# Kernel optimization log

Hardware: AMD Instinct MI355X
Metric: run time of the kernel (lower is better)

The kernel has to match this reference:

```python
import jax, jax.numpy as jnp
import numpy as np

B, N, C = 8, 4096, 64          # graphs, points per graph, feature dim
RATIO = 0.25
M = int(N * RATIO)             # 1024 sampled centroids per graph
R = 0.2                        # radius (points live in the unit cube)
K = 64                         # max_num_neighbors in the forward
BIG = 1e10


def fps_single(pos):
    """Farthest point sampling on one cloud. pos: [N,3] -> [M] local indices.
    Deterministic start at index 0 (PyG uses a random start; math is identical)."""
    n = pos.shape[0]

    def step(carry, _):
        mind, last = carry
        d = jnp.sum((pos - pos[last]) ** 2, axis=-1)      # [N]
        mind = jnp.minimum(mind, d)
        nxt = jnp.argmax(mind)
        return (mind, nxt), nxt

    init = (jnp.full((n,), BIG, pos.dtype), jnp.int32(0))
    _, rest = jax.lax.scan(step, init, None, length=M - 1)
    return jnp.concatenate([jnp.zeros((1,), rest.dtype), rest])


def setup_inputs() -> dict:
    key = jax.random.key(0)
    ks = jax.random.split(key, 8)
    x = jax.random.normal(ks[0], (B * N, C), dtype=jnp.float32)
    pos = jax.random.uniform(ks[1], (B * N, 3), dtype=jnp.float32)
    batch = jnp.repeat(jnp.arange(B, dtype=jnp.int64), N)
    seed_idx = jnp.arange(B * N, dtype=jnp.int64)
    d_in, h, f_out = C + 3, 128, 256
    W1 = jax.random.normal(ks[2], (d_in, h), dtype=jnp.float32) / np.sqrt(d_in)
    b1 = jnp.zeros((h,), jnp.float32)
    W2 = jax.random.normal(ks[3], (h, h), dtype=jnp.float32) / np.sqrt(h)
    b2 = jnp.zeros((h,), jnp.float32)
    W3 = jax.random.normal(ks[4], (h, f_out), dtype=jnp.float32) / np.sqrt(h)
    b3 = jnp.zeros((f_out,), jnp.float32)
    return {"x": x, "pos": pos, "batch": batch, "seed_idx": seed_idx,
            "W1": W1, "b1": b1, "W2": W2, "b2": b2, "W3": W3, "b3": b3}


def reference(x, pos, batch, seed_idx, W1, b1, W2, b2, W3, b3):
    posb = pos.reshape(B, N, 3)
    xb = x.reshape(B, N, C)

    # --- FPS per graph (batch is block-contiguous with N points per graph) ---
    idx_local = jax.vmap(fps_single)(posb)                     # [B, M]
    ctr = jax.vmap(lambda p, i: p[i])(posb, idx_local)         # [B, M, 3]

    # --- radius neighbor search: up to K neighbors within r of each centroid ---
    d2 = jnp.sum((ctr[:, :, None, :] - posb[:, None, :, :]) ** 2, axis=-1)  # [B,M,N]
    d2m = jnp.where(d2 < R * R, d2, BIG)
    neg_d, nbr = jax.lax.top_k(-d2m, K)                        # K nearest within r
    valid = (-neg_d) < R * R                                   # [B, M, K]

    # --- PointConv: msg = MLP([x_j, pos_j - pos_i]), max-aggregate ---
    x_j = jax.vmap(lambda a, i: a[i])(xb, nbr)                 # [B, M, K, C]
    pos_j = jax.vmap(lambda p, i: p[i])(posb, nbr)             # [B, M, K, 3]
    msg = jnp.concatenate([x_j, pos_j - ctr[:, :, None, :]], axis=-1)  # [B,M,K,C+3]
    h = jax.nn.relu(msg @ W1 + b1)
    h = jax.nn.relu(h @ W2 + b2)
    h = jax.nn.relu(h @ W3 + b3)                               # [B, M, K, 256]
    h = jnp.where(valid[..., None], h, -BIG)
    out = jnp.max(h, axis=2)                                   # [B, M, 256]
    out = jnp.where(jnp.any(valid, axis=-1)[..., None], out, 0.0)

    # --- gather sampled outputs back to the flat layout ---
    idx_flat = (idx_local + jnp.arange(B)[:, None] * N).reshape(-1)  # [B*M]
    x_out = out.reshape(B * M, -1)
    pos_out = pos[idx_flat]
    batch_out = batch[idx_flat]
    seed_out = seed_idx[idx_flat]
    return x_out, pos_out, batch_out, seed_out
```

## Files before the change

kernel.cpp:

```cpp
#include <hip/hip_runtime.h>
#include <stdint.h>

#define BB 8
#define NN 4096
#define CC 64
#define MM 1024
#define EE (BB*MM)
#define KK 64
#define F3 256
#define SM 104
#define SH 136
#define CAP 768

typedef __bf16 bf16x8 __attribute__((ext_vector_type(8)));
typedef float floatx4 __attribute__((ext_vector_type(4)));

#define DPP_MAXSTEP(ctrl, rmask) { \
    unsigned o = (unsigned)__builtin_amdgcn_update_dpp(0, (int)v, ctrl, rmask, 0xf, false); \
    v = v > o ? v : o; }
__device__ __forceinline__ unsigned wave_umax_u32(unsigned v) {
  DPP_MAXSTEP(0x111, 0xf)
  DPP_MAXSTEP(0x112, 0xf)
  DPP_MAXSTEP(0x114, 0xf)
  DPP_MAXSTEP(0x118, 0xf)
  DPP_MAXSTEP(0x142, 0xa)
  DPP_MAXSTEP(0x143, 0xc)
  return (unsigned)__builtin_amdgcn_readlane((int)v, 63);
}
#define DPP_MINSTEP(ctrl, rmask) { \
    unsigned o = (unsigned)__builtin_amdgcn_update_dpp((int)0xffffffffu, (int)v, ctrl, rmask, 0xf, false); \
    v = v < o ? v : o; }
__device__ __forceinline__ unsigned wave_umin_u32(unsigned v) {
  DPP_MINSTEP(0x111, 0xf)
  DPP_MINSTEP(0x112, 0xf)
  DPP_MINSTEP(0x114, 0xf)
  DPP_MINSTEP(0x118, 0xf)
  DPP_MINSTEP(0x142, 0xa)
  DPP_MINSTEP(0x143, 0xc)
  return (unsigned)__builtin_amdgcn_readlane((int)v, 63);
}

__device__ __forceinline__ void mlp_item(
    int e, int b, int t,
    const float* __restrict__ x, const float4* __restrict__ pos4,
    const float* __restrict__ ctr, const int* __restrict__ fpsIdx,
    const __bf16* __restrict__ W1t, const __bf16* __restrict__ W2t,
    const __bf16* __restrict__ W3t,
    const float* __restrict__ b1, const float* __restrict__ b2,
    const float* __restrict__ b3,
    float* __restrict__ outX, float* __restrict__ outP,
    float* __restrict__ outB, float* __restrict__ outS,
    __bf16* sMsg, __bf16* sH, int* sSel, int* sCnt) {
  unsigned long long* sDI = (unsigned long long*)sMsg;
  const int lane = t & 63, wv = t >> 6;

  const float cx = ctr[(long)e * 3 + 0];
  const float cy = ctr[(long)e * 3 + 1];
  const float cz = ctr[(long)e * 3 + 2];
  if (t < 3) outP[(long)e * 3 + t] = ctr[(long)e * 3 + t];
  if (t == 3) { outB[e] = (float)b; outS[e] = (float)(b * NN + fpsIdx[e]); }
  const float R2 = (float)(0.2 * 0.2);

#pragma unroll
  for (int q = 0; q < NN / 512; ++q) {
    const int p = t + q * 512;
    const float4 P = pos4[b * NN + p];
    const float dx = __fsub_rn(cx, P.x);
    const float dy = __fsub_rn(cy, P.y);
    const float dz = __fsub_rn(cz, P.z);
    const float d2 = __fadd_rn(__fadd_rn(__fmul_rn(dx, dx), __fmul_rn(dy, dy)), __fmul_rn(dz, dz));
    const bool v = d2 < R2;
    const unsigned long long mask = __ballot(v);
    int wbase = 0;
    if (lane == 0 && mask) wbase = atomicAdd(sCnt, (int)__popcll(mask));
    wbase = __shfl(wbase, 0);
    if (v) {
      const int off = wbase + (int)__popcll(mask & ((1ull << lane) - 1ull));
      if (off < CAP)
        sDI[off] = ((unsigned long long)__float_as_uint(d2) << 32) | (unsigned)p;
    }
  }
  __syncthreads();
  int cnt = *sCnt; cnt = cnt > CAP ? CAP : cnt;
  const int nsel = cnt < KK ? cnt : KK;

  for (int i = t; i < cnt; i += 512) {
    const unsigned long long my = sDI[i];
    int rank = 0;
#pragma unroll 8
    for (int j = 0; j < cnt; ++j) rank += (sDI[j] < my) ? 1 : 0;
    if (rank < KK) sSel[rank] = (int)(unsigned)(my & 0xffffffffu);
  }
  __syncthreads();
  cnt = nsel;

  {
    const int r = t >> 3, p = t & 7;
    float4 a = make_float4(0.f, 0.f, 0.f, 0.f), c4 = a;
    if (r < cnt) {
      const float* xr = x + (long)(b * NN + sSel[r]) * CC + p * 8;
      a  = *(const float4*)xr;
      c4 = *(const float4*)(xr + 4);
    }
    __bf16 o[8] = {(__bf16)a.x, (__bf16)a.y, (__bf16)a.z, (__bf16)a.w,
                   (__bf16)c4.x, (__bf16)c4.y, (__bf16)c4.z, (__bf16)c4.w};
    *(uint4*)&sMsg[r * SM + p * 8] = *(uint4*)o;
  }
  if (t < 64) {
    const int r = t;
    __bf16 d0 = (__bf16)0.0f, d1 = (__bf16)0.0f, d2v = (__bf16)0.0f;
    if (r < cnt) {
      const float4 P = pos4[b * NN + sSel[r]];
      d0  = (__bf16)__fsub_rn(P.x, cx);
      d1  = (__bf16)__fsub_rn(P.y, cy);
      d2v = (__bf16)__fsub_rn(P.z, cz);
    }
    sMsg[r * SM + 64] = d0;
    sMsg[r * SM + 65] = d1;
    sMsg[r * SM + 66] = d2v;
    for (int c = 67; c < SM; ++c) sMsg[r * SM + c] = (__bf16)0.0f;
  }
  __syncthreads();

  const int l15 = lane & 15, quad = lane >> 4;
  {
    floatx4 acc[4] = {};
    const __bf16* wrow = W1t + (wv * 16 + l15) * 96;
#pragma unroll
    for (int ks = 0; ks < 3; ++ks) {
      const bf16x8 bfrag = *(const bf16x8*)(wrow + ks * 32 + quad * 8);
#pragma unroll
      for (int mt = 0; mt < 4; ++mt) {
        const bf16x8 afrag = *(const bf16x8*)&sMsg[(mt * 16 + l15) * SM + ks * 32 + quad * 8];
        acc[mt] = __builtin_amdgcn_mfma_f32_16x16x32_bf16(afrag, bfrag, acc[mt], 0, 0, 0);
      }
    }
    const int col = wv * 16 + l15;
    const float bias = b1[col];
#pragma unroll
    for (int mt = 0; mt < 4; ++mt)
#pragma unroll
      for (int rg = 0; rg < 4; ++rg) {
        const int row = mt * 16 + quad * 4 + rg;
        float v = acc[mt][rg] + bias;
        v = v > 0.0f ? v : 0.0f;
        sH[row * SH + col] = (__bf16)v;
      }
  }
  __syncthreads();
  {
    floatx4 acc[4] = {};
    const __bf16* wrow = W2t + (wv * 16 + l15) * 128;
#pragma unroll
    for (int ks = 0; ks < 4; ++ks) {
      const bf16x8 bfrag = *(const bf16x8*)(wrow + ks * 32 + quad * 8);
#pragma unroll
      for (int mt = 0; mt < 4; ++mt) {
        const bf16x8 afrag = *(const bf16x8*)&sH[(mt * 16 + l15) * SH + ks * 32 + quad * 8];
        acc[mt] = __builtin_amdgcn_mfma_f32_16x16x32_bf16(afrag, bfrag, acc[mt], 0, 0, 0);
      }
    }
    __syncthreads();
    const int col = wv * 16 + l15;
    const float bias = b2[col];
#pragma unroll
    for (int mt = 0; mt < 4; ++mt)
#pragma unroll
      for (int rg = 0; rg < 4; ++rg) {
        const int row = mt * 16 + quad * 4 + rg;
        float v = acc[mt][rg] + bias;
        v = v > 0.0f ? v : 0.0f;
        sH[row * SH + col] = (__bf16)v;
      }
  }
  __syncthreads();
  {
    floatx4 acc[2][4] = {};
#pragma unroll
    for (int ks = 0; ks < 4; ++ks) {
      bf16x8 afrag[4];
#pragma unroll
      for (int mt = 0; mt < 4; ++mt)
        afrag[mt] = *(const bf16x8*)&sH[(mt * 16 + l15) * SH + ks * 32 + quad * 8];
#pragma unroll
      for (int i = 0; i < 2; ++i) {
        const bf16x8 bfrag = *(const bf16x8*)(W3t + ((wv * 2 + i) * 16 + l15) * 128 + ks * 32 + quad * 8);
#pragma unroll
        for (int mt = 0; mt < 4; ++mt)
          acc[i][mt] = __builtin_amdgcn_mfma_f32_16x16x32_bf16(afrag[mt], bfrag, acc[i][mt], 0, 0, 0);
      }
    }
#pragma unroll
    for (int i = 0; i < 2; ++i) {
      const int col = (wv * 2 + i) * 16 + l15;
      const float bias = b3[col];
      float mx = 0.0f;
#pragma unroll
      for (int mt = 0; mt < 4; ++mt)
#pragma unroll
        for (int rg = 0; rg < 4; ++rg) {
          const int row = mt * 16 + quad * 4 + rg;
          float v = acc[i][mt][rg] + bias;
          v = v > 0.0f ? v : 0.0f;
          if (row < cnt) mx = fmaxf(mx, v);
        }
      mx = fmaxf(mx, __shfl_xor(mx, 16));
      mx = fmaxf(mx, __shfl_xor(mx, 32));
      if (quad == 0) outX[(long)e * F3 + col] = mx;
    }
  }
}

#define CTL_PREP 0
#define CTL_PROG(g) (32*((g)+1))
#define CTL_QHEAD 320
#define CTL_DONE 352

__global__ __launch_bounds__(512) void fps_overlap_kernel(
    const float* __restrict__ x, const float* __restrict__ pos,
    const float* __restrict__ W1, const float* __restrict__ b1,
    const float* __restrict__ W2, const float* __restrict__ b2,
    const float* __restrict__ W3, const float* __restrict__ b3,
    int* __restrict__ fpsIdx, float* __restrict__ ctr,
    __bf16* __restrict__ W1t, __bf16* __restrict__ W2t, __bf16* __restrict__ W3t,
    float4* __restrict__ pos4, unsigned* __restrict__ ctl,
    float* __restrict__ outX, float* __restrict__ outP,
    float* __restrict__ outB, float* __restrict__ outS) {
  __shared__ __align__(16) unsigned char sBuf[83968];
  __shared__ int sClaim;

  const int t = threadIdx.x;
  const int blk = blockIdx.x;

  if (blk < BB) {
    const int g = blk;
    float4* sP4 = (float4*)sBuf;
    unsigned long long* sRed = (unsigned long long*)(sBuf + 65536);

    for (int k = g * 11776 + t; k < (g + 1) * 11776; k += 512) {
      if (k < 12288) {
        const int n = k / 96, kk = k % 96;
        W1t[k] = (kk < 67) ? (__bf16)W1[kk * 128 + n] : (__bf16)0.0f;
      } else if (k < 28672) {
        const int i = k - 12288, n = i / 128, kk = i % 128;
        W2t[i] = (__bf16)W2[kk * 128 + n];
      } else if (k < 61440) {
        const int i = k - 28672, n = i / 128, kk = i % 128;
        W3t[i] = (__bf16)W3[kk * 256 + n];
      } else {
        const int i = k - 61440;
        pos4[i] = make_float4(pos[(long)i * 3 + 0], pos[(long)i * 3 + 1],
                              pos[(long)i * 3 + 2], 0.0f);
      }
    }
    __threadfence();
    __syncthreads();
    if (t == 0)
      __hip_atomic_fetch_add(&ctl[CTL_PREP], 1u, __ATOMIC_RELEASE, __HIP_MEMORY_SCOPE_AGENT);

    __builtin_amdgcn_s_setprio(1);

    const int lane = t & 63, wv = t >> 6;
    float px[16], py[16], pz[16], mind[16];
    if (t < 256) {
#pragma unroll
      for (int j = 0; j < 16; ++j) {
        const int p = t + (j << 8);
        const long base = ((long)g * NN + p) * 3;
        px[j] = pos[base + 0];
        py[j] = pos[base + 1];
        pz[j] = pos[base + 2];
        mind[j] = 1e10f;
        sP4[p] = make_float4(px[j], py[j], pz[j], 0.0f);
      }
    }
    __syncthreads();
    float wx = 0.f, wy = 0.f, wz = 0.f;
    if (t < 256) { const float4 w0 = sP4[0]; wx = w0.x; wy = w0.y; wz = w0.z; }
    if (t == 0) {
      const long e0 = (long)g * MM;
      ctr[e0 * 3 + 0] = wx; ctr[e0 * 3 + 1] = wy; ctr[e0 * 3 + 2] = wz;
      fpsIdx[e0] = 0;
    }
    for (int s = 1; s < MM; ++s) {
      if (t < 256) {
        unsigned bb = 0u, bidx = (unsigned)t;
#pragma unroll
        for (int j = 0; j < 16; ++j) {
          const float dx = __fsub_rn(px[j], wx);
          const float dy = __fsub_rn(py[j], wy);
          const float dz = __fsub_rn(pz[j], wz);
          const float d2 = __fadd_rn(__fadd_rn(__fmul_rn(dx, dx), __fmul_rn(dy, dy)), __fmul_rn(dz, dz));
          mind[j] = fminf(mind[j], d2);
          const unsigned mb = __float_as_uint(mind[j]);
          if (mb > bb) { bb = mb; bidx = (unsigned)(t + (j << 8)); }
        }
        const unsigned maxv = wave_umax_u32(bb);
        const unsigned cand = (bb == maxv) ? bidx : 0xffffffffu;
        const unsigned widx_w = wave_umin_u32(cand);
        if (lane == 0)
          sRed[(s & 1) * 4 + wv] = ((unsigned long long)maxv << 32) | (unsigned long long)(~widx_w);
      }
      __asm__ __volatile__("s_waitcnt lgkmcnt(0)" ::: "memory");
      __builtin_amdgcn_s_barrier();
      if (t < 256) {
        unsigned long long m = sRed[(s & 1) * 4 + 0];
#pragma unroll
        for (int w = 1; w < 4; ++w) {
          const unsigned long long o = sRed[(s & 1) * 4 + w];
          m = o > m ? o : m;
        }
        const int widx = (int)(~(unsigned)m);
        const float4 wp = sP4[widx];
        wx = wp.x; wy = wp.y; wz = wp.z;
        if (t == 0) {
          const long eo = (long)g * MM + s;
          ctr[eo * 3 + 0] = wp.x; ctr[eo * 3 + 1] = wp.y; ctr[eo * 3 + 2] = wp.z;
          fpsIdx[eo] = widx;
          if ((s & 63) == 63)
            __hip_atomic_store(&ctl[CTL_PROG(g)], (unsigned)(s + 1),
                               __ATOMIC_RELEASE, __HIP_MEMORY_SCOPE_AGENT);
        }
      }
    }
    __syncthreads();
    if (t == 0) {
      __hip_atomic_store(&ctl[CTL_PROG(g)], 1024u,
                         __ATOMIC_RELEASE, __HIP_MEMORY_SCOPE_AGENT);
      __hip_atomic_fetch_add(&ctl[CTL_DONE], 1u, __ATOMIC_RELEASE, __HIP_MEMORY_SCOPE_AGENT);
    }
    return;
  }

  {
    __bf16* sMsg = (__bf16*)sBuf;
    __bf16* sH   = (__bf16*)(sBuf + 13312);
    int* sSel    = (int*)(sBuf + 30720);
    int* sCnt    = (int*)(sBuf + 30976);

    if (t == 0) {
      while (__hip_atomic_load(&ctl[CTL_PREP], __ATOMIC_ACQUIRE, __HIP_MEMORY_SCOPE_AGENT) < (unsigned)BB)
        __builtin_amdgcn_s_sleep(8);
    }
    __syncthreads();

    for (;;) {
      if (t == 0) {
        unsigned c;
        const unsigned dn = __hip_atomic_load(&ctl[CTL_DONE], __ATOMIC_ACQUIRE, __HIP_MEMORY_SCOPE_AGENT);
        if (dn >= (unsigned)BB) c = EE;
        else c = __hip_atomic_fetch_add(&ctl[CTL_QHEAD], 1u, __ATOMIC_RELAXED, __HIP_MEMORY_SCOPE_AGENT);
        sClaim = (int)c;
      }
      __syncthreads();
      const int c = sClaim;
      if (c >= EE) return;
      const int g = c & 7, sidx = c >> 3;
      const int e = g * MM + sidx;
      if (t == 0) {
        while (__hip_atomic_load(&ctl[CTL_PROG(g)], __ATOMIC_ACQUIRE, __HIP_MEMORY_SCOPE_AGENT)
               <= (unsigned)sidx)
          __builtin_amdgcn_s_sleep(8);
        *sCnt = 0;
      }
      __syncthreads();
      mlp_item(e, g, t, x, pos4, ctr, fpsIdx, W1t, W2t, W3t, b1, b2, b3,
               outX, outP, outB, outS, sMsg, sH, sSel, sCnt);
    }
  }
}

__global__ __launch_bounds__(512) void drain_kernel(
    const float* __restrict__ x, const float4* __restrict__ pos4,
    const float* __restrict__ ctr, const int* __restrict__ fpsIdx,
    const __bf16* __restrict__ W1t, const __bf16* __restrict__ W2t,
    const __bf16* __restrict__ W3t,
    const float* __restrict__ b1, const float* __restrict__ b2,
    const float* __restrict__ b3, unsigned* __restrict__ ctl,
    float* __restrict__ outX, float* __restrict__ outP,
    float* __restrict__ outB, float* __restrict__ outS) {
  __shared__ __align__(16) __bf16 sMsg[64 * SM];
  __shared__ __align__(16) __bf16 sH[64 * SH];
  __shared__ int sSel[KK];
  __shared__ int sCnt;
  __shared__ int sClaim;
  const int t = threadIdx.x;

  if (t == 0) {
    unsigned c = __hip_atomic_load(&ctl[CTL_QHEAD], __ATOMIC_RELAXED, __HIP_MEMORY_SCOPE_AGENT);
    if (c < (unsigned)EE)
      c = __hip_atomic_fetch_add(&ctl[CTL_QHEAD], 1u, __ATOMIC_RELAXED, __HIP_MEMORY_SCOPE_AGENT);
    sClaim = (int)c;
    sCnt = 0;
  }
  __syncthreads();
  const int c = sClaim;
  if (c >= EE) return;
  const int g = c & 7, sidx = c >> 3;
  mlp_item(g * MM + sidx, g, t, x, pos4, ctr, fpsIdx, W1t, W2t, W3t, b1, b2, b3,
           outX, outP, outB, outS, sMsg, sH, sSel, &sCnt);
}

extern "C" void kernel_launch(void* const* d_in, const int* in_sizes, int n_in,
                              void* d_out, int out_size, void* d_ws, size_t ws_size,
                              hipStream_t stream) {
  const float* x   = (const float*)d_in[0];
  const float* pos = (const float*)d_in[1];
  const float* W1  = (const float*)d_in[4];
  const float* b1  = (const float*)d_in[5];
  const float* W2  = (const float*)d_in[6];
  const float* b2  = (const float*)d_in[7];
  const float* W3  = (const float*)d_in[8];
  const float* b3  = (const float*)d_in[9];

  char* ws = (char*)d_ws;
  int*    fpsIdx = (int*)(ws);
  float*  ctr    = (float*)(ws + 32768);
  __bf16* W1t    = (__bf16*)(ws + 131072);
  __bf16* W2t    = (__bf16*)(ws + 155648);
  __bf16* W3t    = (__bf16*)(ws + 188416);
  float4* pos4   = (float4*)(ws + 253952);
  unsigned* ctl  = (unsigned*)(ws + 778240);

  float* outX = (float*)d_out;
  float* outP = outX + (long)EE * F3;
  float* outB = outP + (long)EE * 3;
  float* outS = outB + EE;

  hipMemsetAsync(ctl, 0, 2048, stream);
  fps_overlap_kernel<<<256, 512, 0, stream>>>(x, pos, W1, b1, W2, b2, W3, b3,
                                              fpsIdx, ctr, W1t, W2t, W3t, pos4, ctl,
                                              outX, outP, outB, outS);
  drain_kernel<<<EE, 512, 0, stream>>>(x, pos4, ctr, fpsIdx, W1t, W2t, W3t,
                                       b1, b2, b3, ctl, outX, outP, outB, outS);
}
```

Measured before the change: 817.9 us.

## Run two 512-thread worker teams per 1024-thread block in overlap kernel

The persistent overlap kernel now launches 1024-thread blocks, 8 FPS blocks plus 180 worker blocks. Each worker block splits into two teams with separate shared-memory regions. A block claims two centroid items per queue fetch and each team processes one, putting more concurrent MLP items on each CU. An idle team calls a fixed number of barriers to stay in step with the block-wide syncs inside the item routine. This is fragile if that count ever changes, and the FPS blocks now also run with 1024 threads.

```diff
diff --git a/kernel.cpp b/kernel.cpp
--- a/kernel.cpp
+++ b/kernel.cpp
@@ -11,6 +11,7 @@
 #define SM 104
 #define SH 136
 #define CAP 768
+#define NWORK 180
 
 typedef __bf16 bf16x8 __attribute__((ext_vector_type(8)));
 typedef float floatx4 __attribute__((ext_vector_type(4)));
@@ -41,7 +42,7 @@
 }
 
 __device__ __forceinline__ void mlp_item(
-    int e, int b, int t,
+    int e, int b, int tt,
     const float* __restrict__ x, const float4* __restrict__ pos4,
     const float* __restrict__ ctr, const int* __restrict__ fpsIdx,
     const __bf16* __restrict__ W1t, const __bf16* __restrict__ W2t,
@@ -52,18 +53,18 @@
     float* __restrict__ outB, float* __restrict__ outS,
     __bf16* sMsg, __bf16* sH, int* sSel, int* sCnt) {
   unsigned long long* sDI = (unsigned long long*)sMsg;
-  const int lane = t & 63, wv = t >> 6;
+  const int lane = tt & 63, wv = tt >> 6;
 
   const float cx = ctr[(long)e * 3 + 0];
   const float cy = ctr[(long)e * 3 + 1];
   const float cz = ctr[(long)e * 3 + 2];
-  if (t < 3) outP[(long)e * 3 + t] = ctr[(long)e * 3 + t];
-  if (t == 3) { outB[e] = (float)b; outS[e] = (float)(b * NN + fpsIdx[e]); }
+  if (tt < 3) outP[(long)e * 3 + tt] = ctr[(long)e * 3 + tt];
+  if (tt == 3) { outB[e] = (float)b; outS[e] = (float)(b * NN + fpsIdx[e]); }
   const float R2 = (float)(0.2 * 0.2);
 
 #pragma unroll
   for (int q = 0; q < NN / 512; ++q) {
-    const int p = t + q * 512;
+    const int p = tt + q * 512;
     const float4 P = pos4[b * NN + p];
     const float dx = __fsub_rn(cx, P.x);
     const float dy = __fsub_rn(cy, P.y);
@@ -84,7 +85,7 @@
   int cnt = *sCnt; cnt = cnt > CAP ? CAP : cnt;
   const int nsel = cnt < KK ? cnt : KK;
 
-  for (int i = t; i < cnt; i += 512) {
+  for (int i = tt; i < cnt; i += 512) {
     const unsigned long long my = sDI[i];
     int rank = 0;
 #pragma unroll 8
@@ -95,7 +96,7 @@
   cnt = nsel;
 
   {
-    const int r = t >> 3, p = t & 7;
+    const int r = tt >> 3, p = tt & 7;
     float4 a = make_float4(0.f, 0.f, 0.f, 0.f), c4 = a;
     if (r < cnt) {
       const float* xr = x + (long)(b * NN + sSel[r]) * CC + p * 8;
@@ -106,8 +107,8 @@
                    (__bf16)c4.x, (__bf16)c4.y, (__bf16)c4.z, (__bf16)c4.w};
     *(uint4*)&sMsg[r * SM + p * 8] = *(uint4*)o;
   }
-  if (t < 64) {
-    const int r = t;
+  if (tt < 64) {
+    const int r = tt;
     __bf16 d0 = (__bf16)0.0f, d1 = (__bf16)0.0f, d2v = (__bf16)0.0f;
     if (r < cnt) {
       const float4 P = pos4[b * NN + sSel[r]];
@@ -216,7 +217,7 @@
 #define CTL_QHEAD 320
 #define CTL_DONE 352
 
-__global__ __launch_bounds__(512) void fps_overlap_kernel(
+__global__ __launch_bounds__(1024) void fps_overlap_kernel(
     const float* __restrict__ x, const float* __restrict__ pos,
     const float* __restrict__ W1, const float* __restrict__ b1,
     const float* __restrict__ W2, const float* __restrict__ b2,
@@ -227,7 +228,7 @@
     float* __restrict__ outX, float* __restrict__ outP,
     float* __restrict__ outB, float* __restrict__ outS) {
   __shared__ __align__(16) unsigned char sBuf[83968];
-  __shared__ int sClaim;
+  __shared__ int sClaimA;
 
   const int t = threadIdx.x;
   const int blk = blockIdx.x;
@@ -237,7 +238,7 @@
     float4* sP4 = (float4*)sBuf;
     unsigned long long* sRed = (unsigned long long*)(sBuf + 65536);
 
-    for (int k = g * 11776 + t; k < (g + 1) * 11776; k += 512) {
+    for (int k = g * 11776 + t; k < (g + 1) * 11776; k += 1024) {
       if (k < 12288) {
         const int n = k / 96, kk = k % 96;
         W1t[k] = (kk < 67) ? (__bf16)W1[kk * 128 + n] : (__bf16)0.0f;
@@ -333,10 +334,13 @@
   }
 
   {
-    __bf16* sMsg = (__bf16*)sBuf;
-    __bf16* sH   = (__bf16*)(sBuf + 13312);
-    int* sSel    = (int*)(sBuf + 30720);
-    int* sCnt    = (int*)(sBuf + 30976);
+    const int team = t >> 9;
+    const int tt = t & 511;
+    unsigned char* tb = sBuf + team * 31744;
+    __bf16* sMsg = (__bf16*)tb;
+    __bf16* sH   = (__bf16*)(tb + 13312);
+    int* sSel    = (int*)(tb + 30720);
+    int* sCnt    = (int*)(tb + 30976);
 
     if (t == 0) {
       while (__hip_atomic_load(&ctl[CTL_PREP], __ATOMIC_ACQUIRE, __HIP_MEMORY_SCOPE_AGENT) < (unsigned)BB)
@@ -349,23 +353,30 @@
         unsigned c;
         const unsigned dn = __hip_atomic_load(&ctl[CTL_DONE], __ATOMIC_ACQUIRE, __HIP_MEMORY_SCOPE_AGENT);
         if (dn >= (unsigned)BB) c = EE;
-        else c = __hip_atomic_fetch_add(&ctl[CTL_QHEAD], 1u, __ATOMIC_RELAXED, __HIP_MEMORY_SCOPE_AGENT);
-        sClaim = (int)c;
+        else c = __hip_atomic_fetch_add(&ctl[CTL_QHEAD], 2u, __ATOMIC_RELAXED, __HIP_MEMORY_SCOPE_AGENT);
+        sClaimA = (int)c;
       }
       __syncthreads();
-      const int c = sClaim;
-      if (c >= EE) return;
-      const int g = c & 7, sidx = c >> 3;
+      const int c0 = sClaimA;
+      if (c0 >= EE) return;
+      const int myc = c0 + team;
+      const bool valid = myc < EE;
+      const int g = myc & 7, sidx = (myc >> 3) & (MM - 1);
       const int e = g * MM + sidx;
-      if (t == 0) {
+      if (tt == 0 && valid) {
         while (__hip_atomic_load(&ctl[CTL_PROG(g)], __ATOMIC_ACQUIRE, __HIP_MEMORY_SCOPE_AGENT)
                <= (unsigned)sidx)
           __builtin_amdgcn_s_sleep(8);
         *sCnt = 0;
       }
       __syncthreads();
-      mlp_item(e, g, t, x, pos4, ctr, fpsIdx, W1t, W2t, W3t, b1, b2, b3,
-               outX, outP, outB, outS, sMsg, sH, sSel, sCnt);
+      if (valid) {
+        mlp_item(e, g, tt, x, pos4, ctr, fpsIdx, W1t, W2t, W3t, b1, b2, b3,
+                 outX, outP, outB, outS, sMsg, sH, sSel, sCnt);
+      } else {
+        __syncthreads(); __syncthreads(); __syncthreads();
+        __syncthreads(); __syncthreads(); __syncthreads();
+      }
     }
   }
 }
@@ -428,9 +439,9 @@
   float* outS = outB + EE;
 
   hipMemsetAsync(ctl, 0, 2048, stream);
-  fps_overlap_kernel<<<256, 512, 0, stream>>>(x, pos, W1, b1, W2, b2, W3, b3,
-                                              fpsIdx, ctr, W1t, W2t, W3t, pos4, ctl,
-                                              outX, outP, outB, outS);
+  fps_overlap_kernel<<<BB + NWORK, 1024, 0, stream>>>(x, pos, W1, b1, W2, b2, W3, b3,
+                                                      fpsIdx, ctr, W1t, W2t, W3t, pos4, ctl,
+                                                      outX, outP, outB, outS);
   drain_kernel<<<EE, 512, 0, stream>>>(x, pos4, ctr, fpsIdx, W1t, W2t, W3t,
                                        b1, b2, b3, ctl, outX, outP, outB, outS);
 }
```

Result: no change. 833.0 us (+1.8%).
